# Kernel optimization log

Measured on AMD Instinct MI355X. Metric: run time of the kernel, lower is better.

The kernel has to match this reference:

```python
import jax, jax.numpy as jnp
import numpy as np

D = 1024
H = 16
DH = D // H


def setup_inputs() -> dict:
    key = jax.random.key(0)
    ks = jax.random.split(key, 12)
    s = 0.02
    return {
        "x": jax.random.normal(ks[0], (2, 2048, D), dtype=jnp.float32),
        "ln1_g": jnp.ones((D,), jnp.float32),
        "ln1_b": jnp.zeros((D,), jnp.float32),
        "W_attn": jax.random.normal(ks[1], (3 * D, D), jnp.float32) * s,
        "b_attn": jnp.zeros((3 * D,), jnp.float32),
        "W_proj": jax.random.normal(ks[2], (D, D), jnp.float32) * s,
        "b_proj": jnp.zeros((D,), jnp.float32),
        "ln2_g": jnp.ones((D,), jnp.float32),
        "ln2_b": jnp.zeros((D,), jnp.float32),
        "W_up": jax.random.normal(ks[3], (4 * D, D), jnp.float32) * s,
        "b_up": jnp.zeros((4 * D,), jnp.float32),
        "W_down": jax.random.normal(ks[4], (D, 4 * D), jnp.float32) * s,
        "b_down": jnp.zeros((D,), jnp.float32),
    }


def layernorm(x, g, b, eps=1e-5):
    mu = jnp.mean(x, axis=-1, keepdims=True)
    var = jnp.mean(jnp.square(x - mu), axis=-1, keepdims=True)
    return (x - mu) * jax.lax.rsqrt(var + eps) * g + b


def new_gelu(x):
    c = np.sqrt(2.0 / np.pi).astype(np.float32)
    return 0.5 * x * (1.0 + jnp.tanh(c * (x + 0.044715 * x ** 3)))


def reference(x, ln1_g, ln1_b, W_attn, b_attn, W_proj, b_proj, ln2_g, ln2_b, W_up, b_up, W_down, b_down):
    b, s, d = x.shape
    h = layernorm(x, ln1_g, ln1_b)
    qkv = h @ W_attn.T + b_attn  # [b,s,3d]
    q, k, v = jnp.split(qkv, 3, axis=-1)
    # [b, H, s, DH]
    q = q.reshape(b, s, H, DH).transpose(0, 2, 1, 3)
    k = k.reshape(b, s, H, DH).transpose(0, 2, 1, 3)
    v = v.reshape(b, s, H, DH).transpose(0, 2, 1, 3)
    scores = jnp.einsum("bhqd,bhkd->bhqk", q, k) / np.sqrt(DH).astype(np.float32)
    causal = jnp.tril(jnp.ones((s, s), dtype=bool))
    scores = jnp.where(causal, scores, -jnp.inf)
    attn = jax.nn.softmax(scores, axis=-1)
    o = jnp.einsum("bhqk,bhkd->bhqd", attn, v).transpose(0, 2, 1, 3).reshape(b, s, d)
    x = x + o @ W_proj.T + b_proj
    h2 = layernorm(x, ln2_g, ln2_b)
    mlp = new_gelu(h2 @ W_up.T + b_up) @ W_down.T + b_down
    return x + mlp
```

## Files before the change

### kernel.cpp

```cpp
#include <hip/hip_runtime.h>
#include <hip/hip_bf16.h>

typedef __hip_bfloat16 bf16;
using bf16x8 = __attribute__((ext_vector_type(8))) short;
using bf16x4 = __attribute__((ext_vector_type(4))) short;
using f32x4  = __attribute__((ext_vector_type(4))) float;

#define D_MODEL 1024
#define SEQ     2048
#define NTOK    4096
#define NHEAD   16
#define DHEAD   64

__device__ inline f32x4 mfma16(bf16x8 a, bf16x8 b, f32x4 c) {
  return __builtin_amdgcn_mfma_f32_16x16x32_bf16(a, b, c, 0, 0, 0);
}

__device__ inline f32x4 mfma16k16(bf16x4 a, bf16x4 b, f32x4 c) {
#if __has_builtin(__builtin_amdgcn_mfma_f32_16x16x16bf16_1k)
  return __builtin_amdgcn_mfma_f32_16x16x16bf16_1k(a, b, c, 0, 0, 0);
#else
  f32x4 d;
  asm("v_mfma_f32_16x16x16_bf16 %0, %1, %2, %3" : "=v"(d) : "v"(a), "v"(b), "v"(c));
  return d;
#endif
}

__device__ inline void glds16(const void* g, void* l) {
  __builtin_amdgcn_global_load_lds(
      (const __attribute__((address_space(1))) unsigned int*)g,
      (__attribute__((address_space(3))) unsigned int*)l, 16, 0, 0);
}

__global__ __launch_bounds__(256) void f2bf4_kernel(const float* __restrict__ s0,
                                                    const float* __restrict__ s1,
                                                    const float* __restrict__ s2,
                                                    const float* __restrict__ s3,
                                                    bf16* __restrict__ dst) {
  const size_t M1 = (size_t)D_MODEL * D_MODEL;
  size_t i = ((size_t)blockIdx.x * 256 + threadIdx.x) * 4;
  const float* s; size_t off;
  if (i < 3 * M1)      { s = s0; off = i; }
  else if (i < 4 * M1) { s = s1; off = i - 3 * M1; }
  else if (i < 8 * M1) { s = s2; off = i - 4 * M1; }
  else                 { s = s3; off = i - 8 * M1; }
  float4 v = *(const float4*)(s + off);
  dst[i + 0] = __float2bfloat16(v.x);
  dst[i + 1] = __float2bfloat16(v.y);
  dst[i + 2] = __float2bfloat16(v.z);
  dst[i + 3] = __float2bfloat16(v.w);
}

__global__ __launch_bounds__(256) void ln_kernel(const float* __restrict__ x,
                                                 const float* __restrict__ g,
                                                 const float* __restrict__ bta,
                                                 bf16* __restrict__ out) {
  int row = blockIdx.x;
  int tid = threadIdx.x;
  const float* xr = x + (size_t)row * D_MODEL;
  float4 v = *(const float4*)(xr + tid * 4);
  float s  = v.x + v.y + v.z + v.w;
  float s2 = v.x * v.x + v.y * v.y + v.z * v.z + v.w * v.w;
  for (int o = 32; o > 0; o >>= 1) {
    s  += __shfl_down(s, o);
    s2 += __shfl_down(s2, o);
  }
  __shared__ float red[8];
  int wave = tid >> 6, lane = tid & 63;
  if (lane == 0) { red[wave] = s; red[4 + wave] = s2; }
  __syncthreads();
  s  = red[0] + red[1] + red[2] + red[3];
  s2 = red[4] + red[5] + red[6] + red[7];
  float mu  = s * (1.f / D_MODEL);
  float var = s2 * (1.f / D_MODEL) - mu * mu;
  float rs  = rsqrtf(var + 1e-5f);
  float4 gv = *(const float4*)(g + tid * 4);
  float4 bv = *(const float4*)(bta + tid * 4);
  bf16* orow = out + (size_t)row * D_MODEL + tid * 4;
  orow[0] = __float2bfloat16((v.x - mu) * rs * gv.x + bv.x);
  orow[1] = __float2bfloat16((v.y - mu) * rs * gv.y + bv.y);
  orow[2] = __float2bfloat16((v.z - mu) * rs * gv.z + bv.z);
  orow[3] = __float2bfloat16((v.w - mu) * rs * gv.w + bv.w);
}

#define EP_BIAS_BF16      0
#define EP_BIAS_GELU_BF16 1
#define EP_BIAS_RES_F32   2

template <int EP>
__device__ inline void ep_store(void* out, const float* res, size_t off, float v) {
  if (EP == EP_BIAS_BF16) {
    ((bf16*)out)[off] = __float2bfloat16(v);
  } else if (EP == EP_BIAS_GELU_BF16) {
    float u = 0.7978845608f * (v + 0.044715f * v * v * v);
    float gl = v / (1.0f + __expf(-2.0f * u));
    ((bf16*)out)[off] = __float2bfloat16(gl);
  } else {
    ((float*)out)[off] = res[off] + v;
  }
}

template <int EP>
__global__ __launch_bounds__(256, 3) void gemm_nt(const bf16* __restrict__ A,
                                                  const bf16* __restrict__ W,
                                                  const float* __restrict__ bias,
                                                  const float* res, void* out,
                                                  int M, int N, int K) {
  __shared__ short sA[128 * 64];
  __shared__ short sB[128 * 64];
  int tid  = threadIdx.x;
  int wave = tid >> 6, lane = tid & 63;
  int quad = lane >> 4, l16 = lane & 15;
  int wm = (wave >> 1) * 64, wn = (wave & 1) * 64;
  int bm = blockIdx.x * 128, bn = blockIdx.y * 128;

  int rl = lane >> 3;
  int cz = (lane & 7) ^ rl;
  const bf16* aptr[4];
  const bf16* bptr[4];
#pragma unroll
  for (int i = 0; i < 4; i++) {
    int j = wave * 4 + i;
    aptr[i] = A + (size_t)(bm + j * 8 + rl) * K + cz * 8;
    bptr[i] = W + (size_t)(bn + j * 8 + rl) * K + cz * 8;
  }

  f32x4 acc[4][4] = {};

  for (int k0 = 0; k0 < K; k0 += 64) {
    __syncthreads();
#pragma unroll
    for (int i = 0; i < 4; i++) {
      glds16(aptr[i] + k0, (char*)sA + (wave * 4 + i) * 1024);
      glds16(bptr[i] + k0, (char*)sB + (wave * 4 + i) * 1024);
    }
    __builtin_amdgcn_s_waitcnt(0);
    __syncthreads();

#pragma unroll
    for (int kk = 0; kk < 2; kk++) {
      int cq = kk * 4 + quad;
      int sw = (cq ^ (l16 & 7)) * 8;
      bf16x8 af[4], bfr[4];
#pragma unroll
      for (int t = 0; t < 4; t++) {
        af[t]  = *(const bf16x8*)&sA[(wm + t * 16 + l16) * 64 + sw];
        bfr[t] = *(const bf16x8*)&sB[(wn + t * 16 + l16) * 64 + sw];
      }
#pragma unroll
      for (int mt = 0; mt < 4; mt++)
#pragma unroll
        for (int nt = 0; nt < 4; nt++)
          acc[mt][nt] = mfma16(af[mt], bfr[nt], acc[mt][nt]);
    }
  }

#pragma unroll
  for (int mt = 0; mt < 4; mt++)
#pragma unroll
    for (int nt = 0; nt < 4; nt++) {
      int col = bn + wn + nt * 16 + l16;
      float bs = bias[col];
#pragma unroll
      for (int i = 0; i < 4; i++) {
        int row = bm + wm + mt * 16 + quad * 4 + i;
        ep_store<EP>(out, res, (size_t)row * N + col, acc[mt][nt][i] + bs);
      }
    }
}

template <int EP>
__global__ __launch_bounds__(256, 3) void gemm_nt2(const bf16* __restrict__ A,
                                                   const bf16* __restrict__ W,
                                                   const float* __restrict__ bias,
                                                   const float* res, void* out,
                                                   int M, int N, int K) {
  __shared__ short sA[128 * 64];
  __shared__ short sB[64 * 64];
  int tid  = threadIdx.x;
  int wave = tid >> 6, lane = tid & 63;
  int quad = lane >> 4, l16 = lane & 15;
  int wm = wave * 32;
  int bm = blockIdx.x * 128, bn = blockIdx.y * 64;

  int rl = lane >> 3;
  int cz = (lane & 7) ^ rl;
  const bf16* aptr[4];
  const bf16* bptr[2];
#pragma unroll
  for (int i = 0; i < 4; i++)
    aptr[i] = A + (size_t)(bm + (wave * 4 + i) * 8 + rl) * K + cz * 8;
#pragma unroll
  for (int i = 0; i < 2; i++)
    bptr[i] = W + (size_t)(bn + (wave * 2 + i) * 8 + rl) * K + cz * 8;

  f32x4 acc[2][4] = {};

  for (int k0 = 0; k0 < K; k0 += 64) {
    __syncthreads();
#pragma unroll
    for (int i = 0; i < 4; i++)
      glds16(aptr[i] + k0, (char*)sA + (wave * 4 + i) * 1024);
#pragma unroll
    for (int i = 0; i < 2; i++)
      glds16(bptr[i] + k0, (char*)sB + (wave * 2 + i) * 1024);
    __builtin_amdgcn_s_waitcnt(0);
    __syncthreads();

#pragma unroll
    for (int kk = 0; kk < 2; kk++) {
      int cq = kk * 4 + quad;
      int sw = (cq ^ (l16 & 7)) * 8;
      bf16x8 af[2], bfr[4];
#pragma unroll
      for (int t = 0; t < 2; t++)
        af[t] = *(const bf16x8*)&sA[(wm + t * 16 + l16) * 64 + sw];
#pragma unroll
      for (int t = 0; t < 4; t++)
        bfr[t] = *(const bf16x8*)&sB[(t * 16 + l16) * 64 + sw];
#pragma unroll
      for (int mt = 0; mt < 2; mt++)
#pragma unroll
        for (int nt = 0; nt < 4; nt++)
          acc[mt][nt] = mfma16(af[mt], bfr[nt], acc[mt][nt]);
    }
  }

#pragma unroll
  for (int mt = 0; mt < 2; mt++)
#pragma unroll
    for (int nt = 0; nt < 4; nt++) {
      int col = bn + nt * 16 + l16;
      float bs = bias[col];
#pragma unroll
      for (int i = 0; i < 4; i++) {
        int row = bm + wm + mt * 16 + quad * 4 + i;
        ep_store<EP>(out, res, (size_t)row * N + col, acc[mt][nt][i] + bs);
      }
    }
}

__global__ __launch_bounds__(256, 2) void attn_kernel(const short* __restrict__ qkvS,
                                                      short* __restrict__ oS) {
  int bh = blockIdx.y;
  int b = bh >> 4, h = bh & 15;
  int iq = blockIdx.x;
  int qa = iq * 64, qb = (31 - iq) * 64;
  int tid = threadIdx.x, wave = tid >> 6, lane = tid & 63;
  int quad = lane >> 4, l16 = lane & 15;
  const int RS = 3 * D_MODEL;
  const short* base = qkvS + (size_t)b * SEQ * RS;
  const int koff = D_MODEL + h * 64, voff = 2 * D_MODEL + h * 64, qoff = h * 64;
  const float c2 = 0.1803368801f;

  __shared__ short sK[64 * 64];
  __shared__ short sV[64 * 64];

  int rl = lane >> 3, cz = (lane & 7) ^ rl;
  int vkr = tid >> 3, vd0 = (tid & 7) * 8;
  int vb7 = tid & 7;
  int kv3 = vkr & 3;
  int c4lo = vkr >> 2, c4hi = c4lo + 8;
  int xpar = (c4lo & 1) << 3;

  int qrA = qa + wave * 16 + l16, qrB = qb + wave * 16 + l16;
  bf16x8 qA0 = *(const bf16x8*)&base[(size_t)qrA * RS + qoff + quad * 8];
  bf16x8 qA1 = *(const bf16x8*)&base[(size_t)qrA * RS + qoff + 32 + quad * 8];
  bf16x8 qB0 = *(const bf16x8*)&base[(size_t)qrB * RS + qoff + quad * 8];
  bf16x8 qB1 = *(const bf16x8*)&base[(size_t)qrB * RS + qoff + 32 + quad * 8];

  f32x4 oA[4] = {}, oB[4] = {};
  float lsA = 0.f, lsB = 0.f;
  int ntile = 32 - iq;

  bf16x8 kc0, kc1, vc0, vc1;
  {
    const short* kp = &base[(size_t)(wave * 16 + rl) * RS + koff + cz * 8];
    kc0 = *(const bf16x8*)kp;
    kc1 = *(const bf16x8*)(kp + (size_t)8 * RS);
    const short* vp = &base[(size_t)vkr * RS + voff + vd0];
    vc0 = *(const bf16x8*)vp;
    vc1 = *(const bf16x8*)(vp + (size_t)32 * RS);
  }

  auto ptail = [&](const f32x4* st, f32x4* oo, float& ls, bool diag, int qg, int kv0) {
#pragma unroll
    for (int t16 = 0; t16 < 4; t16++) {
      bf16x4 pf;
      int kvb = kv0 + t16 * 16 + quad * 4;
#pragma unroll
      for (int e = 0; e < 4; e++) {
        float p = exp2f(fminf(st[t16][e] * c2, 30.f));
        if (diag && (kvb + e > qg)) p = 0.f;
        ls += p;
        pf[e] = __builtin_bit_cast(short, __float2bfloat16(p));
      }
      int c4r = t16 * 4 + quad;
      int xr = (c4r & 1) << 3;
#pragma unroll
      for (int dt = 0; dt < 4; dt++) {
        int pr = (dt * 16 + l16) ^ xr;
        bf16x4 vb = *(const bf16x4*)&sV[c4r * 256 + pr * 4];
        oo[dt] = mfma16k16(pf, vb, oo[dt]);
      }
    }
  };

  for (int t = 0; t < ntile; t++) {
    int kv0 = t * 64;
    asm volatile("s_waitcnt lgkmcnt(0)" ::: "memory");
    asm volatile("s_barrier" ::: "memory");

    bf16x8 kn0, kn1, vn0, vn1;
    bool more = (t + 1 < ntile);
    if (more) {
      int kvn = kv0 + 64;
      const short* kp = &base[(size_t)(kvn + wave * 16 + rl) * RS + koff + cz * 8];
      kn0 = *(const bf16x8*)kp;
      kn1 = *(const bf16x8*)(kp + (size_t)8 * RS);
      const short* vp = &base[(size_t)(kvn + vkr) * RS + voff + vd0];
      vn0 = *(const bf16x8*)vp;
      vn1 = *(const bf16x8*)(vp + (size_t)32 * RS);
    }

    *(bf16x8*)&sK[(wave * 2 + 0) * 512 + lane * 8] = kc0;
    *(bf16x8*)&sK[(wave * 2 + 1) * 512 + lane * 8] = kc1;
#pragma unroll
    for (int j = 0; j < 8; j++)
      sV[c4lo * 256 + (vb7 | ((j << 3) ^ xpar)) * 4 + kv3] = vc0[j];
#pragma unroll
    for (int j = 0; j < 8; j++)
      sV[c4hi * 256 + (vb7 | ((j << 3) ^ xpar)) * 4 + kv3] = vc1[j];

    asm volatile("s_waitcnt lgkmcnt(0)" ::: "memory");
    asm volatile("s_barrier" ::: "memory");

    bool doA = (t <= iq);
    int xk = l16 & 7;
    f32x4 stB[4], stA[4];
#pragma unroll
    for (int t16 = 0; t16 < 4; t16++) {
      bf16x8 kf0 = *(const bf16x8*)&sK[(t16 * 16 + l16) * 64 + ((quad ^ xk) * 8)];
      bf16x8 kf1 = *(const bf16x8*)&sK[(t16 * 16 + l16) * 64 + (((quad + 4) ^ xk) * 8)];
      f32x4 z = {};
      z = mfma16(kf0, qB0, z);
      stB[t16] = mfma16(kf1, qB1, z);
      if (doA) {
        f32x4 za = {};
        za = mfma16(kf0, qA0, za);
        stA[t16] = mfma16(kf1, qA1, za);
      }
    }
    ptail(stB, oB, lsB, t == ntile - 1, qb + wave * 16 + l16, kv0);
    if (doA) ptail(stA, oA, lsA, t == iq, qa + wave * 16 + l16, kv0);

    if (more) { kc0 = kn0; kc1 = kn1; vc0 = vn0; vc1 = vn1; }
  }

  auto finish = [&](f32x4* oo, float ls, int q0p) {
    ls += __shfl_xor(ls, 16);
    ls += __shfl_xor(ls, 32);
    float inv[4];
#pragma unroll
    for (int e = 0; e < 4; e++) inv[e] = 1.0f / __shfl(ls, quad * 4 + e);
    int sigbase = ((l16 & 7) << 3) | (l16 >> 3);
#pragma unroll
    for (int dt = 0; dt < 4; dt++)
#pragma unroll
      for (int e = 0; e < 4; e++) {
        int row = q0p + wave * 16 + quad * 4 + e;
        oS[((size_t)b * SEQ + row) * D_MODEL + qoff + sigbase + dt * 2] =
            __builtin_bit_cast(short, __float2bfloat16(oo[dt][e] * inv[e]));
      }
  };
  finish(oB, lsB, qb);
  finish(oA, lsA, qa);
}

extern "C" void kernel_launch(void* const* d_in, const int* in_sizes, int n_in,
                              void* d_out, int out_size, void* d_ws, size_t ws_size,
                              hipStream_t stream) {
  const float* x      = (const float*)d_in[0];
  const float* ln1_g  = (const float*)d_in[1];
  const float* ln1_b  = (const float*)d_in[2];
  const float* W_attn = (const float*)d_in[3];
  const float* b_attn = (const float*)d_in[4];
  const float* W_proj = (const float*)d_in[5];
  const float* b_proj = (const float*)d_in[6];
  const float* ln2_g  = (const float*)d_in[7];
  const float* ln2_b  = (const float*)d_in[8];
  const float* W_up   = (const float*)d_in[9];
  const float* b_up   = (const float*)d_in[10];
  const float* W_down = (const float*)d_in[11];
  const float* b_down = (const float*)d_in[12];
  float* out = (float*)d_out;

  char* p = (char*)d_ws;
  bf16* Wattn_b = (bf16*)p; p += (size_t)3 * D_MODEL * D_MODEL * 2;
  bf16* Wproj_b = (bf16*)p; p += (size_t)D_MODEL * D_MODEL * 2;
  bf16* Wup_b   = (bf16*)p; p += (size_t)4 * D_MODEL * D_MODEL * 2;
  bf16* Wdown_b = (bf16*)p; p += (size_t)4 * D_MODEL * D_MODEL * 2;
  bf16* h_b     = (bf16*)p; p += (size_t)NTOK * D_MODEL * 2;
  bf16* qkv_b   = (bf16*)p; p += (size_t)NTOK * 3 * D_MODEL * 2;
  bf16* o_b     = (bf16*)p; p += (size_t)NTOK * D_MODEL * 2;
  bf16* h2_b    = (bf16*)p; p += (size_t)NTOK * D_MODEL * 2;
  bf16* up_b    = (bf16*)p; p += (size_t)NTOK * 4 * D_MODEL * 2;

  {
    size_t ntot = (size_t)12 * D_MODEL * D_MODEL;
    f2bf4_kernel<<<(int)(ntot / 1024), 256, 0, stream>>>(W_attn, W_proj, W_up, W_down, Wattn_b);
  }
  ln_kernel<<<NTOK, 256, 0, stream>>>(x, ln1_g, ln1_b, h_b);
  gemm_nt<EP_BIAS_BF16><<<dim3(NTOK / 128, 3 * D_MODEL / 128), 256, 0, stream>>>(
      h_b, Wattn_b, b_attn, nullptr, qkv_b, NTOK, 3 * D_MODEL, D_MODEL);
  attn_kernel<<<dim3(16, 2 * NHEAD), 256, 0, stream>>>((const short*)qkv_b, (short*)o_b);
  gemm_nt2<EP_BIAS_RES_F32><<<dim3(NTOK / 128, D_MODEL / 64), 256, 0, stream>>>(
      o_b, Wproj_b, b_proj, x, out, NTOK, D_MODEL, D_MODEL);
  ln_kernel<<<NTOK, 256, 0, stream>>>(out, ln2_g, ln2_b, h2_b);
  gemm_nt<EP_BIAS_GELU_BF16><<<dim3(NTOK / 128, 4 * D_MODEL / 128), 256, 0, stream>>>(
      h2_b, Wup_b, b_up, nullptr, up_b, NTOK, 4 * D_MODEL, D_MODEL);
  gemm_nt2<EP_BIAS_RES_F32><<<dim3(NTOK / 128, D_MODEL / 64), 256, 0, stream>>>(
      up_b, Wdown_b, b_down, out, out, NTOK, D_MODEL, 4 * D_MODEL);
}
```

Measured before the change: 356.3 us.

## Register-prefetch GEMM tiles and split attention into one q-tile per block

Both GEMM kernels drop direct global-to-LDS loads. They now prefetch the next K tile into registers while the current tile is computed, then store it to LDS between barriers, with occupancy hints lowered from 3 to 2. This hides global load latency instead of waiting on every tile. The attention kernel no longer pairs a short and a long causal q-tile per block. It launches 32 blocks per head, each handling one q-tile, with heaviest tiles scheduled first. This raises parallelism but drops the built-in load balancing and uses more registers for the prefetch buffers.

After: 371.8 us. +4.4%, slower.

```diff
diff --git a/kernel.cpp b/kernel.cpp
--- a/kernel.cpp
+++ b/kernel.cpp
@@ -26,11 +26,9 @@
 #endif
 }
 
-__device__ inline void glds16(const void* g, void* l) {
-  __builtin_amdgcn_global_load_lds(
-      (const __attribute__((address_space(1))) unsigned int*)g,
-      (__attribute__((address_space(3))) unsigned int*)l, 16, 0, 0);
-}
+#define LGKM0_BARRIER()                                        \
+  asm volatile("s_waitcnt lgkmcnt(0)" ::: "memory");           \
+  asm volatile("s_barrier" ::: "memory")
 
 __global__ __launch_bounds__(256) void f2bf4_kernel(const float* __restrict__ s0,
                                                     const float* __restrict__ s1,
@@ -101,13 +99,15 @@
 }
 
 template <int EP>
-__global__ __launch_bounds__(256, 3) void gemm_nt(const bf16* __restrict__ A,
-                                                  const bf16* __restrict__ W,
+__global__ __launch_bounds__(256, 2) void gemm_nt(const bf16* __restrict__ A_,
+                                                  const bf16* __restrict__ W_,
                                                   const float* __restrict__ bias,
                                                   const float* res, void* out,
                                                   int M, int N, int K) {
   __shared__ short sA[128 * 64];
   __shared__ short sB[128 * 64];
+  const short* A = (const short*)A_;
+  const short* W = (const short*)W_;
   int tid  = threadIdx.x;
   int wave = tid >> 6, lane = tid & 63;
   int quad = lane >> 4, l16 = lane & 15;
@@ -116,26 +116,41 @@
 
   int rl = lane >> 3;
   int cz = (lane & 7) ^ rl;
-  const bf16* aptr[4];
-  const bf16* bptr[4];
+  const short* ap[4];
+  const short* bp[4];
 #pragma unroll
   for (int i = 0; i < 4; i++) {
     int j = wave * 4 + i;
-    aptr[i] = A + (size_t)(bm + j * 8 + rl) * K + cz * 8;
-    bptr[i] = W + (size_t)(bn + j * 8 + rl) * K + cz * 8;
+    ap[i] = A + (size_t)(bm + j * 8 + rl) * K + cz * 8;
+    bp[i] = W + (size_t)(bn + j * 8 + rl) * K + cz * 8;
+  }
+
+  bf16x8 ac[4], bc[4];
+#pragma unroll
+  for (int i = 0; i < 4; i++) {
+    ac[i] = *(const bf16x8*)ap[i];
+    bc[i] = *(const bf16x8*)bp[i];
   }
 
   f32x4 acc[4][4] = {};
 
   for (int k0 = 0; k0 < K; k0 += 64) {
-    __syncthreads();
+    bool more = (k0 + 64 < K);
+    bf16x8 an[4], bn4[4];
+    if (more) {
+#pragma unroll
+      for (int i = 0; i < 4; i++) {
+        an[i]  = *(const bf16x8*)(ap[i] + k0 + 64);
+        bn4[i] = *(const bf16x8*)(bp[i] + k0 + 64);
+      }
+    }
+    LGKM0_BARRIER();
 #pragma unroll
     for (int i = 0; i < 4; i++) {
-      glds16(aptr[i] + k0, (char*)sA + (wave * 4 + i) * 1024);
-      glds16(bptr[i] + k0, (char*)sB + (wave * 4 + i) * 1024);
-    }
-    __builtin_amdgcn_s_waitcnt(0);
-    __syncthreads();
+      *(bf16x8*)&sA[(wave * 4 + i) * 512 + lane * 8] = ac[i];
+      *(bf16x8*)&sB[(wave * 4 + i) * 512 + lane * 8] = bc[i];
+    }
+    LGKM0_BARRIER();
 
 #pragma unroll
     for (int kk = 0; kk < 2; kk++) {
@@ -153,6 +168,10 @@
         for (int nt = 0; nt < 4; nt++)
           acc[mt][nt] = mfma16(af[mt], bfr[nt], acc[mt][nt]);
     }
+    if (more) {
+#pragma unroll
+      for (int i = 0; i < 4; i++) { ac[i] = an[i]; bc[i] = bn4[i]; }
+    }
   }
 
 #pragma unroll
@@ -170,13 +189,15 @@
 }
 
 template <int EP>
-__global__ __launch_bounds__(256, 3) void gemm_nt2(const bf16* __restrict__ A,
-                                                   const bf16* __restrict__ W,
+__global__ __launch_bounds__(256, 2) void gemm_nt2(const bf16* __restrict__ A_,
+                                                   const bf16* __restrict__ W_,
                                                    const float* __restrict__ bias,
                                                    const float* res, void* out,
                                                    int M, int N, int K) {
   __shared__ short sA[128 * 64];
   __shared__ short sB[64 * 64];
+  const short* A = (const short*)A_;
+  const short* W = (const short*)W_;
   int tid  = threadIdx.x;
   int wave = tid >> 6, lane = tid & 63;
   int quad = lane >> 4, l16 = lane & 15;
@@ -185,27 +206,40 @@
 
   int rl = lane >> 3;
   int cz = (lane & 7) ^ rl;
-  const bf16* aptr[4];
-  const bf16* bptr[2];
+  const short* ap[4];
+  const short* bp[2];
 #pragma unroll
   for (int i = 0; i < 4; i++)
-    aptr[i] = A + (size_t)(bm + (wave * 4 + i) * 8 + rl) * K + cz * 8;
+    ap[i] = A + (size_t)(bm + (wave * 4 + i) * 8 + rl) * K + cz * 8;
 #pragma unroll
   for (int i = 0; i < 2; i++)
-    bptr[i] = W + (size_t)(bn + (wave * 2 + i) * 8 + rl) * K + cz * 8;
+    bp[i] = W + (size_t)(bn + (wave * 2 + i) * 8 + rl) * K + cz * 8;
+
+  bf16x8 ac[4], bc[2];
+#pragma unroll
+  for (int i = 0; i < 4; i++) ac[i] = *(const bf16x8*)ap[i];
+#pragma unroll
+  for (int i = 0; i < 2; i++) bc[i] = *(const bf16x8*)bp[i];
 
   f32x4 acc[2][4] = {};
 
   for (int k0 = 0; k0 < K; k0 += 64) {
-    __syncthreads();
+    bool more = (k0 + 64 < K);
+    bf16x8 an[4], bn4[2];
+    if (more) {
+#pragma unroll
+      for (int i = 0; i < 4; i++) an[i]  = *(const bf16x8*)(ap[i] + k0 + 64);
+#pragma unroll
+      for (int i = 0; i < 2; i++) bn4[i] = *(const bf16x8*)(bp[i] + k0 + 64);
+    }
+    LGKM0_BARRIER();
 #pragma unroll
     for (int i = 0; i < 4; i++)
-      glds16(aptr[i] + k0, (char*)sA + (wave * 4 + i) * 1024);
+      *(bf16x8*)&sA[(wave * 4 + i) * 512 + lane * 8] = ac[i];
 #pragma unroll
     for (int i = 0; i < 2; i++)
-      glds16(bptr[i] + k0, (char*)sB + (wave * 2 + i) * 1024);
-    __builtin_amdgcn_s_waitcnt(0);
-    __syncthreads();
+      *(bf16x8*)&sB[(wave * 2 + i) * 512 + lane * 8] = bc[i];
+    LGKM0_BARRIER();
 
 #pragma unroll
     for (int kk = 0; kk < 2; kk++) {
@@ -224,6 +258,12 @@
         for (int nt = 0; nt < 4; nt++)
           acc[mt][nt] = mfma16(af[mt], bfr[nt], acc[mt][nt]);
     }
+    if (more) {
+#pragma unroll
+      for (int i = 0; i < 4; i++) ac[i] = an[i];
+#pragma unroll
+      for (int i = 0; i < 2; i++) bc[i] = bn4[i];
+    }
   }
 
 #pragma unroll
@@ -244,8 +284,9 @@
                                                       short* __restrict__ oS) {
   int bh = blockIdx.y;
   int b = bh >> 4, h = bh & 15;
-  int iq = blockIdx.x;
-  int qa = iq * 64, qb = (31 - iq) * 64;
+  int qi = 31 - (int)blockIdx.x;
+  int q0 = qi * 64;
+  int ntile = qi + 1;
   int tid = threadIdx.x, wave = tid >> 6, lane = tid & 63;
   int quad = lane >> 4, l16 = lane & 15;
   const int RS = 3 * D_MODEL;
@@ -263,15 +304,12 @@
   int c4lo = vkr >> 2, c4hi = c4lo + 8;
   int xpar = (c4lo & 1) << 3;
 
-  int qrA = qa + wave * 16 + l16, qrB = qb + wave * 16 + l16;
-  bf16x8 qA0 = *(const bf16x8*)&base[(size_t)qrA * RS + qoff + quad * 8];
-  bf16x8 qA1 = *(const bf16x8*)&base[(size_t)qrA * RS + qoff + 32 + quad * 8];
-  bf16x8 qB0 = *(const bf16x8*)&base[(size_t)qrB * RS + qoff + quad * 8];
-  bf16x8 qB1 = *(const bf16x8*)&base[(size_t)qrB * RS + qoff + 32 + quad * 8];
-
-  f32x4 oA[4] = {}, oB[4] = {};
-  float lsA = 0.f, lsB = 0.f;
-  int ntile = 32 - iq;
+  int qr = q0 + wave * 16 + l16;
+  bf16x8 qf0 = *(const bf16x8*)&base[(size_t)qr * RS + qoff + quad * 8];
+  bf16x8 qf1 = *(const bf16x8*)&base[(size_t)qr * RS + qoff + 32 + quad * 8];
+
+  f32x4 oacc[4] = {};
+  float ls = 0.f;
 
   bf16x8 kc0, kc1, vc0, vc1;
   {
@@ -283,33 +321,9 @@
     vc1 = *(const bf16x8*)(vp + (size_t)32 * RS);
   }
 
-  auto ptail = [&](const f32x4* st, f32x4* oo, float& ls, bool diag, int qg, int kv0) {
-#pragma unroll
-    for (int t16 = 0; t16 < 4; t16++) {
-      bf16x4 pf;
-      int kvb = kv0 + t16 * 16 + quad * 4;
-#pragma unroll
-      for (int e = 0; e < 4; e++) {
-        float p = exp2f(fminf(st[t16][e] * c2, 30.f));
-        if (diag && (kvb + e > qg)) p = 0.f;
-        ls += p;
-        pf[e] = __builtin_bit_cast(short, __float2bfloat16(p));
-      }
-      int c4r = t16 * 4 + quad;
-      int xr = (c4r & 1) << 3;
-#pragma unroll
-      for (int dt = 0; dt < 4; dt++) {
-        int pr = (dt * 16 + l16) ^ xr;
-        bf16x4 vb = *(const bf16x4*)&sV[c4r * 256 + pr * 4];
-        oo[dt] = mfma16k16(pf, vb, oo[dt]);
-      }
-    }
-  };
-
   for (int t = 0; t < ntile; t++) {
     int kv0 = t * 64;
-    asm volatile("s_waitcnt lgkmcnt(0)" ::: "memory");
-    asm volatile("s_barrier" ::: "memory");
+    LGKM0_BARRIER();
 
     bf16x8 kn0, kn1, vn0, vn1;
     bool more = (t + 1 < ntile);
@@ -332,49 +346,58 @@
     for (int j = 0; j < 8; j++)
       sV[c4hi * 256 + (vb7 | ((j << 3) ^ xpar)) * 4 + kv3] = vc1[j];
 
-    asm volatile("s_waitcnt lgkmcnt(0)" ::: "memory");
-    asm volatile("s_barrier" ::: "memory");
-
-    bool doA = (t <= iq);
+    LGKM0_BARRIER();
+
     int xk = l16 & 7;
-    f32x4 stB[4], stA[4];
+    f32x4 st[4];
 #pragma unroll
     for (int t16 = 0; t16 < 4; t16++) {
       bf16x8 kf0 = *(const bf16x8*)&sK[(t16 * 16 + l16) * 64 + ((quad ^ xk) * 8)];
       bf16x8 kf1 = *(const bf16x8*)&sK[(t16 * 16 + l16) * 64 + (((quad + 4) ^ xk) * 8)];
       f32x4 z = {};
-      z = mfma16(kf0, qB0, z);
-      stB[t16] = mfma16(kf1, qB1, z);
-      if (doA) {
-        f32x4 za = {};
-        za = mfma16(kf0, qA0, za);
-        stA[t16] = mfma16(kf1, qA1, za);
-      }
-    }
-    ptail(stB, oB, lsB, t == ntile - 1, qb + wave * 16 + l16, kv0);
-    if (doA) ptail(stA, oA, lsA, t == iq, qa + wave * 16 + l16, kv0);
+      z = mfma16(kf0, qf0, z);
+      st[t16] = mfma16(kf1, qf1, z);
+    }
+
+    bool diag = (t == ntile - 1);
+#pragma unroll
+    for (int t16 = 0; t16 < 4; t16++) {
+      bf16x4 pf;
+      int kvb = kv0 + t16 * 16 + quad * 4;
+#pragma unroll
+      for (int e = 0; e < 4; e++) {
+        float p = exp2f(fminf(st[t16][e] * c2, 30.f));
+        if (diag && (kvb + e > qr)) p = 0.f;
+        ls += p;
+        pf[e] = __builtin_bit_cast(short, __float2bfloat16(p));
+      }
+      int c4r = t16 * 4 + quad;
+      int xr = (c4r & 1) << 3;
+#pragma unroll
+      for (int dt = 0; dt < 4; dt++) {
+        int pr = (dt * 16 + l16) ^ xr;
+        bf16x4 vb = *(const bf16x4*)&sV[c4r * 256 + pr * 4];
+        oacc[dt] = mfma16k16(pf, vb, oacc[dt]);
+      }
+    }
 
     if (more) { kc0 = kn0; kc1 = kn1; vc0 = vn0; vc1 = vn1; }
   }
 
-  auto finish = [&](f32x4* oo, float ls, int q0p) {
-    ls += __shfl_xor(ls, 16);
-    ls += __shfl_xor(ls, 32);
-    float inv[4];
-#pragma unroll
-    for (int e = 0; e < 4; e++) inv[e] = 1.0f / __shfl(ls, quad * 4 + e);
-    int sigbase = ((l16 & 7) << 3) | (l16 >> 3);
-#pragma unroll
-    for (int dt = 0; dt < 4; dt++)
-#pragma unroll
-      for (int e = 0; e < 4; e++) {
-        int row = q0p + wave * 16 + quad * 4 + e;
-        oS[((size_t)b * SEQ + row) * D_MODEL + qoff + sigbase + dt * 2] =
-            __builtin_bit_cast(short, __float2bfloat16(oo[dt][e] * inv[e]));
-      }
-  };
-  finish(oB, lsB, qb);
-  finish(oA, lsA, qa);
+  ls += __shfl_xor(ls, 16);
+  ls += __shfl_xor(ls, 32);
+  float inv[4];
+#pragma unroll
+  for (int e = 0; e < 4; e++) inv[e] = 1.0f / __shfl(ls, quad * 4 + e);
+  int sigbase = ((l16 & 7) << 3) | (l16 >> 3);
+#pragma unroll
+  for (int dt = 0; dt < 4; dt++)
+#pragma unroll
+    for (int e = 0; e < 4; e++) {
+      int row = q0 + wave * 16 + quad * 4 + e;
+      oS[((size_t)b * SEQ + row) * D_MODEL + qoff + sigbase + dt * 2] =
+          __builtin_bit_cast(short, __float2bfloat16(oacc[dt][e] * inv[e]));
+    }
 }
 
 extern "C" void kernel_launch(void* const* d_in, const int* in_sizes, int n_in,
@@ -413,7 +436,7 @@
   ln_kernel<<<NTOK, 256, 0, stream>>>(x, ln1_g, ln1_b, h_b);
   gemm_nt<EP_BIAS_BF16><<<dim3(NTOK / 128, 3 * D_MODEL / 128), 256, 0, stream>>>(
       h_b, Wattn_b, b_attn, nullptr, qkv_b, NTOK, 3 * D_MODEL, D_MODEL);
-  attn_kernel<<<dim3(16, 2 * NHEAD), 256, 0, stream>>>((const short*)qkv_b, (short*)o_b);
+  attn_kernel<<<dim3(32, 2 * NHEAD), 256, 0, stream>>>((const short*)qkv_b, (short*)o_b);
   gemm_nt2<EP_BIAS_RES_F32><<<dim3(NTOK / 128, D_MODEL / 64), 256, 0, stream>>>(
       o_b, Wproj_b, b_proj, x, out, NTOK, D_MODEL, D_MODEL);
   ln_kernel<<<NTOK, 256, 0, stream>>>(out, ln2_g, ln2_b, h2_b);
```

## Double-buffer weight tiles in LDS and stream activations directly into registers

Applied to the files above, without the earlier changes.

Both GEMM kernels now keep the A operand out of LDS. Each lane loads its MFMA fragments straight from global memory into registers and prefetches the next K-step into a second register set. The B tile is double-buffered in LDS, and the next tile's async global-to-LDS copy is issued before the current tile's MFMAs, using a partial vmcnt wait instead of a full drain. This aims to overlap global loads with compute and halve LDS traffic, at the cost of more VGPRs and less coalesced A reads. The attention kernel's ptail lambda is only moved inside the loop and its barrier code macro-ized.

After: 434.9 us. +22.1%, slower.

```diff
diff --git a/kernel.cpp b/kernel.cpp
--- a/kernel.cpp
+++ b/kernel.cpp
@@ -31,6 +31,11 @@
       (const __attribute__((address_space(1))) unsigned int*)g,
       (__attribute__((address_space(3))) unsigned int*)l, 16, 0, 0);
 }
+
+#define MEMFENCE() asm volatile("" ::: "memory")
+#define LGKM0_BARRIER()                                        \
+  asm volatile("s_waitcnt lgkmcnt(0)" ::: "memory");           \
+  asm volatile("s_barrier" ::: "memory")
 
 __global__ __launch_bounds__(256) void f2bf4_kernel(const float* __restrict__ s0,
                                                     const float* __restrict__ s1,
@@ -101,57 +106,82 @@
 }
 
 template <int EP>
-__global__ __launch_bounds__(256, 3) void gemm_nt(const bf16* __restrict__ A,
-                                                  const bf16* __restrict__ W,
+__global__ __launch_bounds__(256, 3) void gemm_nt(const bf16* __restrict__ A_,
+                                                  const bf16* __restrict__ W_,
                                                   const float* __restrict__ bias,
                                                   const float* res, void* out,
                                                   int M, int N, int K) {
-  __shared__ short sA[128 * 64];
-  __shared__ short sB[128 * 64];
+  __shared__ short sB[2][128 * 64];
+  const short* A = (const short*)A_;
+  const short* W = (const short*)W_;
   int tid  = threadIdx.x;
   int wave = tid >> 6, lane = tid & 63;
   int quad = lane >> 4, l16 = lane & 15;
   int wm = (wave >> 1) * 64, wn = (wave & 1) * 64;
   int bm = blockIdx.x * 128, bn = blockIdx.y * 128;
 
-  int rl = lane >> 3;
-  int cz = (lane & 7) ^ rl;
-  const bf16* aptr[4];
-  const bf16* bptr[4];
-#pragma unroll
-  for (int i = 0; i < 4; i++) {
-    int j = wave * 4 + i;
-    aptr[i] = A + (size_t)(bm + j * 8 + rl) * K + cz * 8;
-    bptr[i] = W + (size_t)(bn + j * 8 + rl) * K + cz * 8;
-  }
+  int rl = lane >> 3, cz = (lane & 7) ^ rl;
+  const short* bp[4];
+#pragma unroll
+  for (int i = 0; i < 4; i++)
+    bp[i] = W + (size_t)(bn + (wave * 4 + i) * 8 + rl) * K + cz * 8;
+  const short* ar[4];
+#pragma unroll
+  for (int t = 0; t < 4; t++)
+    ar[t] = A + (size_t)(bm + wm + t * 16 + l16) * K + quad * 8;
+
+#pragma unroll
+  for (int i = 0; i < 4; i++)
+    glds16(bp[i], (char*)sB[0] + (wave * 4 + i) * 1024);
+  MEMFENCE();
+  bf16x8 acur[4][2], anext[4][2];
+#pragma unroll
+  for (int t = 0; t < 4; t++)
+#pragma unroll
+    for (int kk = 0; kk < 2; kk++)
+      acur[t][kk] = *(const bf16x8*)(ar[t] + kk * 32);
 
   f32x4 acc[4][4] = {};
-
-  for (int k0 = 0; k0 < K; k0 += 64) {
-    __syncthreads();
-#pragma unroll
-    for (int i = 0; i < 4; i++) {
-      glds16(aptr[i] + k0, (char*)sA + (wave * 4 + i) * 1024);
-      glds16(bptr[i] + k0, (char*)sB + (wave * 4 + i) * 1024);
-    }
-    __builtin_amdgcn_s_waitcnt(0);
-    __syncthreads();
-
+  int niter = K >> 6;
+
+  for (int it = 0; it < niter; it++) {
+    int k0 = it << 6;
+    asm volatile("s_waitcnt vmcnt(8)" ::: "memory");
+    LGKM0_BARRIER();
+
+    bool more = (it + 1 < niter);
+    if (more) {
+#pragma unroll
+      for (int i = 0; i < 4; i++)
+        glds16(bp[i] + k0 + 64, (char*)sB[(it + 1) & 1] + (wave * 4 + i) * 1024);
+      MEMFENCE();
+#pragma unroll
+      for (int t = 0; t < 4; t++)
+#pragma unroll
+        for (int kk = 0; kk < 2; kk++)
+          anext[t][kk] = *(const bf16x8*)(ar[t] + k0 + 64 + kk * 32);
+    }
+
+    const short* sb = sB[it & 1];
 #pragma unroll
     for (int kk = 0; kk < 2; kk++) {
-      int cq = kk * 4 + quad;
-      int sw = (cq ^ (l16 & 7)) * 8;
-      bf16x8 af[4], bfr[4];
-#pragma unroll
-      for (int t = 0; t < 4; t++) {
-        af[t]  = *(const bf16x8*)&sA[(wm + t * 16 + l16) * 64 + sw];
-        bfr[t] = *(const bf16x8*)&sB[(wn + t * 16 + l16) * 64 + sw];
-      }
+      int sw = (((kk * 4 + quad)) ^ (l16 & 7)) * 8;
+      bf16x8 bfr[4];
+#pragma unroll
+      for (int t = 0; t < 4; t++)
+        bfr[t] = *(const bf16x8*)&sb[(wn + t * 16 + l16) * 64 + sw];
 #pragma unroll
       for (int mt = 0; mt < 4; mt++)
 #pragma unroll
         for (int nt = 0; nt < 4; nt++)
-          acc[mt][nt] = mfma16(af[mt], bfr[nt], acc[mt][nt]);
+          acc[mt][nt] = mfma16(acur[mt][kk], bfr[nt], acc[mt][nt]);
+    }
+    if (more) {
+#pragma unroll
+      for (int t = 0; t < 4; t++)
+#pragma unroll
+        for (int kk = 0; kk < 2; kk++)
+          acur[t][kk] = anext[t][kk];
     }
   }
 
@@ -170,59 +200,82 @@
 }
 
 template <int EP>
-__global__ __launch_bounds__(256, 3) void gemm_nt2(const bf16* __restrict__ A,
-                                                   const bf16* __restrict__ W,
+__global__ __launch_bounds__(256, 3) void gemm_nt2(const bf16* __restrict__ A_,
+                                                   const bf16* __restrict__ W_,
                                                    const float* __restrict__ bias,
                                                    const float* res, void* out,
                                                    int M, int N, int K) {
-  __shared__ short sA[128 * 64];
-  __shared__ short sB[64 * 64];
+  __shared__ short sB[2][64 * 64];
+  const short* A = (const short*)A_;
+  const short* W = (const short*)W_;
   int tid  = threadIdx.x;
   int wave = tid >> 6, lane = tid & 63;
   int quad = lane >> 4, l16 = lane & 15;
   int wm = wave * 32;
   int bm = blockIdx.x * 128, bn = blockIdx.y * 64;
 
-  int rl = lane >> 3;
-  int cz = (lane & 7) ^ rl;
-  const bf16* aptr[4];
-  const bf16* bptr[2];
-#pragma unroll
-  for (int i = 0; i < 4; i++)
-    aptr[i] = A + (size_t)(bm + (wave * 4 + i) * 8 + rl) * K + cz * 8;
+  int rl = lane >> 3, cz = (lane & 7) ^ rl;
+  const short* bp[2];
 #pragma unroll
   for (int i = 0; i < 2; i++)
-    bptr[i] = W + (size_t)(bn + (wave * 2 + i) * 8 + rl) * K + cz * 8;
+    bp[i] = W + (size_t)(bn + (wave * 2 + i) * 8 + rl) * K + cz * 8;
+  const short* ar[2];
+#pragma unroll
+  for (int t = 0; t < 2; t++)
+    ar[t] = A + (size_t)(bm + wm + t * 16 + l16) * K + quad * 8;
+
+#pragma unroll
+  for (int i = 0; i < 2; i++)
+    glds16(bp[i], (char*)sB[0] + (wave * 2 + i) * 1024);
+  MEMFENCE();
+  bf16x8 acur[2][2], anext[2][2];
+#pragma unroll
+  for (int t = 0; t < 2; t++)
+#pragma unroll
+    for (int kk = 0; kk < 2; kk++)
+      acur[t][kk] = *(const bf16x8*)(ar[t] + kk * 32);
 
   f32x4 acc[2][4] = {};
-
-  for (int k0 = 0; k0 < K; k0 += 64) {
-    __syncthreads();
-#pragma unroll
-    for (int i = 0; i < 4; i++)
-      glds16(aptr[i] + k0, (char*)sA + (wave * 4 + i) * 1024);
-#pragma unroll
-    for (int i = 0; i < 2; i++)
-      glds16(bptr[i] + k0, (char*)sB + (wave * 2 + i) * 1024);
-    __builtin_amdgcn_s_waitcnt(0);
-    __syncthreads();
-
+  int niter = K >> 6;
+
+  for (int it = 0; it < niter; it++) {
+    int k0 = it << 6;
+    asm volatile("s_waitcnt vmcnt(4)" ::: "memory");
+    LGKM0_BARRIER();
+
+    bool more = (it + 1 < niter);
+    if (more) {
+#pragma unroll
+      for (int i = 0; i < 2; i++)
+        glds16(bp[i] + k0 + 64, (char*)sB[(it + 1) & 1] + (wave * 2 + i) * 1024);
+      MEMFENCE();
+#pragma unroll
+      for (int t = 0; t < 2; t++)
+#pragma unroll
+        for (int kk = 0; kk < 2; kk++)
+          anext[t][kk] = *(const bf16x8*)(ar[t] + k0 + 64 + kk * 32);
+    }
+
+    const short* sb = sB[it & 1];
 #pragma unroll
     for (int kk = 0; kk < 2; kk++) {
-      int cq = kk * 4 + quad;
-      int sw = (cq ^ (l16 & 7)) * 8;
-      bf16x8 af[2], bfr[4];
+      int sw = (((kk * 4 + quad)) ^ (l16 & 7)) * 8;
+      bf16x8 bfr[4];
+#pragma unroll
+      for (int t = 0; t < 4; t++)
+        bfr[t] = *(const bf16x8*)&sb[(t * 16 + l16) * 64 + sw];
+#pragma unroll
+      for (int mt = 0; mt < 2; mt++)
+#pragma unroll
+        for (int nt = 0; nt < 4; nt++)
+          acc[mt][nt] = mfma16(acur[mt][kk], bfr[nt], acc[mt][nt]);
+    }
+    if (more) {
 #pragma unroll
       for (int t = 0; t < 2; t++)
-        af[t] = *(const bf16x8*)&sA[(wm + t * 16 + l16) * 64 + sw];
-#pragma unroll
-      for (int t = 0; t < 4; t++)
-        bfr[t] = *(const bf16x8*)&sB[(t * 16 + l16) * 64 + sw];
-#pragma unroll
-      for (int mt = 0; mt < 2; mt++)
-#pragma unroll
-        for (int nt = 0; nt < 4; nt++)
-          acc[mt][nt] = mfma16(af[mt], bfr[nt], acc[mt][nt]);
+#pragma unroll
+        for (int kk = 0; kk < 2; kk++)
+          acur[t][kk] = anext[t][kk];
     }
   }
 
@@ -283,33 +336,9 @@
     vc1 = *(const bf16x8*)(vp + (size_t)32 * RS);
   }
 
-  auto ptail = [&](const f32x4* st, f32x4* oo, float& ls, bool diag, int qg, int kv0) {
-#pragma unroll
-    for (int t16 = 0; t16 < 4; t16++) {
-      bf16x4 pf;
-      int kvb = kv0 + t16 * 16 + quad * 4;
-#pragma unroll
-      for (int e = 0; e < 4; e++) {
-        float p = exp2f(fminf(st[t16][e] * c2, 30.f));
-        if (diag && (kvb + e > qg)) p = 0.f;
-        ls += p;
-        pf[e] = __builtin_bit_cast(short, __float2bfloat16(p));
-      }
-      int c4r = t16 * 4 + quad;
-      int xr = (c4r & 1) << 3;
-#pragma unroll
-      for (int dt = 0; dt < 4; dt++) {
-        int pr = (dt * 16 + l16) ^ xr;
-        bf16x4 vb = *(const bf16x4*)&sV[c4r * 256 + pr * 4];
-        oo[dt] = mfma16k16(pf, vb, oo[dt]);
-      }
-    }
-  };
-
   for (int t = 0; t < ntile; t++) {
     int kv0 = t * 64;
-    asm volatile("s_waitcnt lgkmcnt(0)" ::: "memory");
-    asm volatile("s_barrier" ::: "memory");
+    LGKM0_BARRIER();
 
     bf16x8 kn0, kn1, vn0, vn1;
     bool more = (t + 1 < ntile);
@@ -332,8 +361,7 @@
     for (int j = 0; j < 8; j++)
       sV[c4hi * 256 + (vb7 | ((j << 3) ^ xpar)) * 4 + kv3] = vc1[j];
 
-    asm volatile("s_waitcnt lgkmcnt(0)" ::: "memory");
-    asm volatile("s_barrier" ::: "memory");
+    LGKM0_BARRIER();
 
     bool doA = (t <= iq);
     int xk = l16 & 7;
@@ -351,8 +379,32 @@
         stA[t16] = mfma16(kf1, qA1, za);
       }
     }
-    ptail(stB, oB, lsB, t == ntile - 1, qb + wave * 16 + l16, kv0);
-    if (doA) ptail(stA, oA, lsA, t == iq, qa + wave * 16 + l16, kv0);
+
+    auto ptail = [&](const f32x4* st, f32x4* oo, float& ls, bool diag, int qg) {
+#pragma unroll
+      for (int t16 = 0; t16 < 4; t16++) {
+        bf16x4 pf;
+        int kvb = kv0 + t16 * 16 + quad * 4;
+#pragma unroll
+        for (int e = 0; e < 4; e++) {
+          float p = exp2f(fminf(st[t16][e] * c2, 30.f));
+          if (diag && (kvb + e > qg)) p = 0.f;
+          ls += p;
+          pf[e] = __builtin_bit_cast(short, __float2bfloat16(p));
+        }
+        int c4r = t16 * 4 + quad;
+        int xr = (c4r & 1) << 3;
+#pragma unroll
+        for (int dt = 0; dt < 4; dt++) {
+          int pr = (dt * 16 + l16) ^ xr;
+          bf16x4 vb = *(const bf16x4*)&sV[c4r * 256 + pr * 4];
+          oo[dt] = mfma16k16(pf, vb, oo[dt]);
+        }
+      }
+    };
+
+    ptail(stB, oB, lsB, t == ntile - 1, qrB);
+    if (doA) ptail(stA, oA, lsA, t == iq, qrA);
 
     if (more) { kc0 = kn0; kc1 = kn1; vc0 = vn0; vc1 = vn1; }
   }
```
